# Performance work log

Measured on AMD Instinct MI355X. Metric: run time of the kernel, lower is better.

The kernel has to match this reference:

```python
import jax, jax.numpy as jnp
import numpy as np

B, N, H, V = 64, 640, 768, 50265
LN_EPS = 1e-5


def setup_inputs() -> dict:
    key = jax.random.key(0)
    ks = jax.random.split(key, 12)
    inputs = jax.random.randint(ks[0], (B, N), 0, V)
    position_idx = jax.random.randint(ks[1], (B, N), 0, 10)
    attn_mask = jax.random.randint(ks[2], (B, N, N), 0, 2).astype(bool)
    s = 0.02
    emb_table = jax.random.normal(ks[3], (V, H), jnp.float32) * s
    pooler_w = jax.random.normal(ks[4], (H, H), jnp.float32) * s
    pooler_b = jnp.zeros((H,), jnp.float32)
    dense_w = jax.random.normal(ks[5], (H, H), jnp.float32) * s
    dense_b = jnp.zeros((H,), jnp.float32)
    ln_g = jnp.ones((H,), jnp.float32)
    ln_b = jnp.zeros((H,), jnp.float32)
    dec_w = jax.random.normal(ks[6], (H, 1), jnp.float32) * s
    dec_b = jnp.zeros((1,), jnp.float32)
    return {
        'inputs': inputs, 'position_idx': position_idx, 'attn_mask': attn_mask,
        'emb_table': emb_table, 'pooler_w': pooler_w, 'pooler_b': pooler_b,
        'dense_w': dense_w, 'dense_b': dense_b, 'ln_g': ln_g, 'ln_b': ln_b,
        'dec_w': dec_w, 'dec_b': dec_b,
    }


def _layer_norm(x, g, b):
    mu = jnp.mean(x, axis=-1, keepdims=True)
    var = jnp.mean(jnp.square(x - mu), axis=-1, keepdims=True)
    return (x - mu) * jax.lax.rsqrt(var + LN_EPS) * g + b


def reference(inputs, position_idx, attn_mask, emb_table, pooler_w, pooler_b,
              dense_w, dense_b, ln_g, ln_b, dec_w, dec_b):
    nodes_mask = position_idx == 0            # [B,N] DFG nodes
    token_mask = position_idx >= 2            # [B,N] code tokens
    emb = emb_table[inputs]                   # [B,N,H] word embedding gather
    # node->token adjacency, then row-normalize (broadcast AND fused into float mul)
    m = (nodes_mask[:, :, None] & token_mask[:, None, :] & attn_mask).astype(emb.dtype)
    m = m / (jnp.sum(m, axis=-1, keepdims=True) + 1e-10)
    avg = jnp.einsum('bnm,bmd->bnd', m, emb)  # masked mean of token embs per node
    nm = nodes_mask[:, :, None].astype(emb.dtype)
    emb = emb * (1.0 - nm) + avg * nm
    # encoder stand-in: RoBERTa pooler (dense+tanh on first position) of aggregated embeddings
    pooled = jnp.tanh(emb[:, 0] @ pooler_w + pooler_b)   # [B,H]
    # RobertaLMHead
    x = jax.nn.gelu(pooled @ dense_w + dense_b, approximate=False)
    x = _layer_norm(x, ln_g, ln_b)
    x = x @ dec_w + dec_b                                # [B,1]
    return jnp.tanh(x)
```

## Files before the change

### kernel.cpp

```cpp
#include <hip/hip_runtime.h>
#include <cstdint>

#define B_SZ 64
#define N_SZ 640
#define H_SZ 768
#define NCHUNK 32
#define CHUNK (N_SZ / NCHUNK)
#define LN_EPS 1e-5f

__global__ void k_embed_partial(const int* __restrict__ inputs,
                                const int* __restrict__ pos,
                                const int* __restrict__ amask,
                                const float* __restrict__ emb,
                                float* __restrict__ partials,
                                float* __restrict__ counts) {
    const int c   = blockIdx.x;
    const int b   = blockIdx.y;
    const int tid = threadIdx.x;

    if (pos[b * N_SZ] != 0) return;

    __shared__ float wgt[CHUNK];
    __shared__ int   rowid[CHUNK];
    if (tid < CHUNK) {
        const int m = c * CHUNK + tid;
        const int active = (pos[b * N_SZ + m] >= 2) &&
                           (amask[(size_t)b * N_SZ * N_SZ + m] != 0);
        wgt[tid]   = active ? 1.0f : 0.0f;
        rowid[tid] = inputs[b * N_SZ + m];
    }
    __syncthreads();

    float a0 = 0.f, a1 = 0.f, a2 = 0.f;
#pragma unroll 5
    for (int m = 0; m < CHUNK; ++m) {
        const float  w   = wgt[m];
        const size_t row = (size_t)rowid[m] * H_SZ;
        a0 = fmaf(w, emb[row + tid],       a0);
        a1 = fmaf(w, emb[row + tid + 256], a1);
        a2 = fmaf(w, emb[row + tid + 512], a2);
    }
    float* pout = partials + ((size_t)b * NCHUNK + c) * H_SZ;
    pout[tid]       = a0;
    pout[tid + 256] = a1;
    pout[tid + 512] = a2;
    if (tid == 0) {
        float s = 0.f;
        for (int m = 0; m < CHUNK; ++m) s += wgt[m];
        counts[b * NCHUNK + c] = s;
    }
}

__global__ void k_embed_reduce(const int* __restrict__ inputs,
                               const int* __restrict__ pos,
                               const float* __restrict__ emb,
                               const float* __restrict__ partials,
                               const float* __restrict__ counts,
                               float* __restrict__ e0) {
    const int b   = blockIdx.x;
    const int tid = threadIdx.x;

    if (pos[b * N_SZ] != 0) {
        const size_t row = (size_t)inputs[b * N_SZ] * H_SZ;
        for (int h = tid; h < H_SZ; h += 256)
            e0[b * H_SZ + h] = emb[row + h];
        return;
    }

    float cnt = 0.f;
    for (int c = 0; c < NCHUNK; ++c) cnt += counts[b * NCHUNK + c];
    const float scale = 1.0f / (cnt + 1e-10f);

    float a0 = 0.f, a1 = 0.f, a2 = 0.f;
    const float* p = partials + (size_t)b * NCHUNK * H_SZ;
#pragma unroll 8
    for (int c = 0; c < NCHUNK; ++c) {
        a0 += p[c * H_SZ + tid];
        a1 += p[c * H_SZ + tid + 256];
        a2 += p[c * H_SZ + tid + 512];
    }
    e0[b * H_SZ + tid]       = a0 * scale;
    e0[b * H_SZ + tid + 256] = a1 * scale;
    e0[b * H_SZ + tid + 512] = a2 * scale;
}

template <int ACT>
__global__ void k_gemv(const float* __restrict__ x,
                       const float* __restrict__ w,
                       const float* __restrict__ bias,
                       float* __restrict__ y) {
    const int b = blockIdx.y;
    const int j = blockIdx.x * 256 + threadIdx.x;
    __shared__ float xs[H_SZ];
    for (int h = threadIdx.x; h < H_SZ; h += 256)
        xs[h] = x[b * H_SZ + h];
    __syncthreads();

    float acc = 0.f;
#pragma unroll 8
    for (int k = 0; k < H_SZ; ++k)
        acc = fmaf(xs[k], w[k * H_SZ + j], acc);
    acc += bias[j];
    if (ACT == 0) {
        acc = tanhf(acc);
    } else {
        acc = acc * 0.5f * (1.0f + erff(acc * 0.70710678118654752f));
    }
    y[b * H_SZ + j] = acc;
}

__global__ void k_final(const float* __restrict__ x,
                        const float* __restrict__ g,
                        const float* __restrict__ beta,
                        const float* __restrict__ dw,
                        const float* __restrict__ db,
                        float* __restrict__ out) {
    const int b    = blockIdx.x;
    const int tid  = threadIdx.x;
    const int lane = tid & 63;
    const int wave = tid >> 6;
    __shared__ float red[8];

    const float v0 = x[b * H_SZ + tid];
    const float v1 = x[b * H_SZ + tid + 256];
    const float v2 = x[b * H_SZ + tid + 512];

    float s = v0 + v1 + v2;
    for (int o = 32; o > 0; o >>= 1) s += __shfl_down(s, o, 64);
    if (lane == 0) red[wave] = s;
    __syncthreads();
    if (tid == 0) red[0] = red[0] + red[1] + red[2] + red[3];
    __syncthreads();
    const float mean = red[0] * (1.0f / H_SZ);
    __syncthreads();

    const float d0 = v0 - mean, d1 = v1 - mean, d2 = v2 - mean;
    float q = d0 * d0 + d1 * d1 + d2 * d2;
    for (int o = 32; o > 0; o >>= 1) q += __shfl_down(q, o, 64);
    if (lane == 0) red[wave] = q;
    __syncthreads();
    if (tid == 0) red[0] = red[0] + red[1] + red[2] + red[3];
    __syncthreads();
    const float rstd = rsqrtf(red[0] * (1.0f / H_SZ) + LN_EPS);
    __syncthreads();

    float p = 0.f;
    p += (d0 * rstd * g[tid]       + beta[tid])       * dw[tid];
    p += (d1 * rstd * g[tid + 256] + beta[tid + 256]) * dw[tid + 256];
    p += (d2 * rstd * g[tid + 512] + beta[tid + 512]) * dw[tid + 512];
    for (int o = 32; o > 0; o >>= 1) p += __shfl_down(p, o, 64);
    if (lane == 0) red[wave] = p;
    __syncthreads();
    if (tid == 0)
        out[b] = tanhf(red[0] + red[1] + red[2] + red[3] + db[0]);
}

extern "C" void kernel_launch(void* const* d_in, const int* in_sizes, int n_in,
                              void* d_out, int out_size, void* d_ws, size_t ws_size,
                              hipStream_t stream) {
    const int*   inputs = (const int*)d_in[0];
    const int*   pos    = (const int*)d_in[1];
    const int*   amask  = (const int*)d_in[2];
    const float* emb    = (const float*)d_in[3];
    const float* pw     = (const float*)d_in[4];
    const float* pb     = (const float*)d_in[5];
    const float* dw     = (const float*)d_in[6];
    const float* db     = (const float*)d_in[7];
    const float* lg     = (const float*)d_in[8];
    const float* lb     = (const float*)d_in[9];
    const float* decw   = (const float*)d_in[10];
    const float* decb   = (const float*)d_in[11];
    float* out = (float*)d_out;

    float* partials = (float*)d_ws;
    float* counts   = partials + (size_t)B_SZ * NCHUNK * H_SZ;
    float* e0       = counts + B_SZ * NCHUNK;
    float* pooled   = e0 + B_SZ * H_SZ;
    float* xb       = pooled + B_SZ * H_SZ;

    k_embed_partial<<<dim3(NCHUNK, B_SZ), 256, 0, stream>>>(inputs, pos, amask, emb,
                                                            partials, counts);
    k_embed_reduce<<<B_SZ, 256, 0, stream>>>(inputs, pos, emb, partials, counts, e0);
    k_gemv<0><<<dim3(3, B_SZ), 256, 0, stream>>>(e0, pw, pb, pooled);
    k_gemv<1><<<dim3(3, B_SZ), 256, 0, stream>>>(pooled, dw, db, xb);
    k_final<<<B_SZ, 256, 0, stream>>>(xb, lg, lb, decw, decb, out);
}
```

Before: 94.23 us.

## Fuse embed-reduce into pooler, fuse GELU-GEMV with LayerNorm head, batch two rows per block

```diff
diff --git a/kernel.cpp b/kernel.cpp
--- a/kernel.cpp
+++ b/kernel.cpp
@@ -32,7 +32,7 @@
     __syncthreads();
 
     float a0 = 0.f, a1 = 0.f, a2 = 0.f;
-#pragma unroll 5
+#pragma unroll 10
     for (int m = 0; m < CHUNK; ++m) {
         const float  w   = wgt[m];
         const size_t row = (size_t)rowid[m] * H_SZ;
@@ -51,108 +51,119 @@
     }
 }
 
-__global__ void k_embed_reduce(const int* __restrict__ inputs,
-                               const int* __restrict__ pos,
-                               const float* __restrict__ emb,
-                               const float* __restrict__ partials,
-                               const float* __restrict__ counts,
-                               float* __restrict__ e0) {
-    const int b   = blockIdx.x;
-    const int tid = threadIdx.x;
-
-    if (pos[b * N_SZ] != 0) {
-        const size_t row = (size_t)inputs[b * N_SZ] * H_SZ;
-        for (int h = tid; h < H_SZ; h += 256)
-            e0[b * H_SZ + h] = emb[row + h];
-        return;
+__device__ __forceinline__ float2 block_sum2(float2 v, float2* red2, int tid) {
+    const int lane = tid & 63;
+    const int wave = tid >> 6;
+    for (int o = 32; o > 0; o >>= 1) {
+        v.x += __shfl_down(v.x, o, 64);
+        v.y += __shfl_down(v.y, o, 64);
     }
-
-    float cnt = 0.f;
-    for (int c = 0; c < NCHUNK; ++c) cnt += counts[b * NCHUNK + c];
-    const float scale = 1.0f / (cnt + 1e-10f);
-
-    float a0 = 0.f, a1 = 0.f, a2 = 0.f;
-    const float* p = partials + (size_t)b * NCHUNK * H_SZ;
-#pragma unroll 8
-    for (int c = 0; c < NCHUNK; ++c) {
-        a0 += p[c * H_SZ + tid];
-        a1 += p[c * H_SZ + tid + 256];
-        a2 += p[c * H_SZ + tid + 512];
+    if (lane == 0) red2[wave] = v;
+    __syncthreads();
+    if (tid == 0) {
+        float2 s = make_float2(0.f, 0.f);
+        for (int i = 0; i < 12; ++i) { s.x += red2[i].x; s.y += red2[i].y; }
+        red2[0] = s;
     }
-    e0[b * H_SZ + tid]       = a0 * scale;
-    e0[b * H_SZ + tid + 256] = a1 * scale;
-    e0[b * H_SZ + tid + 512] = a2 * scale;
+    __syncthreads();
+    const float2 s = red2[0];
+    __syncthreads();
+    return s;
 }
 
-template <int ACT>
-__global__ void k_gemv(const float* __restrict__ x,
-                       const float* __restrict__ w,
-                       const float* __restrict__ bias,
-                       float* __restrict__ y) {
-    const int b = blockIdx.y;
-    const int j = blockIdx.x * 256 + threadIdx.x;
-    __shared__ float xs[H_SZ];
-    for (int h = threadIdx.x; h < H_SZ; h += 256)
-        xs[h] = x[b * H_SZ + h];
+__global__ __launch_bounds__(768) void k_pooler(const int* __restrict__ inputs,
+                                                const int* __restrict__ pos,
+                                                const float* __restrict__ emb,
+                                                const float* __restrict__ partials,
+                                                const float* __restrict__ counts,
+                                                const float* __restrict__ pw,
+                                                const float* __restrict__ pb,
+                                                float* __restrict__ pooled) {
+    const int b0 = blockIdx.x * 2;
+    const int j  = threadIdx.x;
+    __shared__ float2 xs[H_SZ];
+
+    float v[2];
+#pragma unroll
+    for (int p = 0; p < 2; ++p) {
+        const int b = b0 + p;
+        if (pos[b * N_SZ] != 0) {
+            v[p] = emb[(size_t)inputs[b * N_SZ] * H_SZ + j];
+        } else {
+            float cnt = 0.f;
+            for (int c = 0; c < NCHUNK; ++c) cnt += counts[b * NCHUNK + c];
+            const float scale = 1.0f / (cnt + 1e-10f);
+            float a = 0.f;
+            const float* pp = partials + (size_t)b * NCHUNK * H_SZ + j;
+#pragma unroll 8
+            for (int c = 0; c < NCHUNK; ++c) a += pp[(size_t)c * H_SZ];
+            v[p] = a * scale;
+        }
+    }
+    xs[j] = make_float2(v[0], v[1]);
     __syncthreads();
 
-    float acc = 0.f;
+    float acc0 = 0.f, acc1 = 0.f;
 #pragma unroll 8
-    for (int k = 0; k < H_SZ; ++k)
-        acc = fmaf(xs[k], w[k * H_SZ + j], acc);
-    acc += bias[j];
-    if (ACT == 0) {
-        acc = tanhf(acc);
-    } else {
-        acc = acc * 0.5f * (1.0f + erff(acc * 0.70710678118654752f));
+    for (int k = 0; k < H_SZ; ++k) {
+        const float  wv = pw[k * H_SZ + j];
+        const float2 xv = xs[k];
+        acc0 = fmaf(wv, xv.x, acc0);
+        acc1 = fmaf(wv, xv.y, acc1);
     }
-    y[b * H_SZ + j] = acc;
+    const float bj = pb[j];
+    pooled[(size_t)b0 * H_SZ + j]       = tanhf(acc0 + bj);
+    pooled[(size_t)(b0 + 1) * H_SZ + j] = tanhf(acc1 + bj);
 }
 
-__global__ void k_final(const float* __restrict__ x,
-                        const float* __restrict__ g,
-                        const float* __restrict__ beta,
-                        const float* __restrict__ dw,
-                        const float* __restrict__ db,
-                        float* __restrict__ out) {
-    const int b    = blockIdx.x;
-    const int tid  = threadIdx.x;
-    const int lane = tid & 63;
-    const int wave = tid >> 6;
-    __shared__ float red[8];
+__global__ __launch_bounds__(768) void k_lmhead(const float* __restrict__ pooled,
+                                                const float* __restrict__ dwm,
+                                                const float* __restrict__ dbv,
+                                                const float* __restrict__ lg,
+                                                const float* __restrict__ lb,
+                                                const float* __restrict__ decw,
+                                                const float* __restrict__ decb,
+                                                float* __restrict__ out) {
+    const int b0 = blockIdx.x * 2;
+    const int j  = threadIdx.x;
+    __shared__ float2 xs[H_SZ];
+    __shared__ float2 red2[12];
 
-    const float v0 = x[b * H_SZ + tid];
-    const float v1 = x[b * H_SZ + tid + 256];
-    const float v2 = x[b * H_SZ + tid + 512];
-
-    float s = v0 + v1 + v2;
-    for (int o = 32; o > 0; o >>= 1) s += __shfl_down(s, o, 64);
-    if (lane == 0) red[wave] = s;
-    __syncthreads();
-    if (tid == 0) red[0] = red[0] + red[1] + red[2] + red[3];
-    __syncthreads();
-    const float mean = red[0] * (1.0f / H_SZ);
+    xs[j] = make_float2(pooled[(size_t)b0 * H_SZ + j],
+                        pooled[(size_t)(b0 + 1) * H_SZ + j]);
     __syncthreads();
 
-    const float d0 = v0 - mean, d1 = v1 - mean, d2 = v2 - mean;
-    float q = d0 * d0 + d1 * d1 + d2 * d2;
-    for (int o = 32; o > 0; o >>= 1) q += __shfl_down(q, o, 64);
-    if (lane == 0) red[wave] = q;
-    __syncthreads();
-    if (tid == 0) red[0] = red[0] + red[1] + red[2] + red[3];
-    __syncthreads();
-    const float rstd = rsqrtf(red[0] * (1.0f / H_SZ) + LN_EPS);
+    float acc0 = 0.f, acc1 = 0.f;
+#pragma unroll 8
+    for (int k = 0; k < H_SZ; ++k) {
+        const float  wv = dwm[k * H_SZ + j];
+        const float2 xv = xs[k];
+        acc0 = fmaf(wv, xv.x, acc0);
+        acc1 = fmaf(wv, xv.y, acc1);
+    }
+    const float bj = dbv[j];
+    acc0 += bj; acc1 += bj;
+    const float g0 = acc0 * 0.5f * (1.0f + erff(acc0 * 0.70710678118654752f));
+    const float g1 = acc1 * 0.5f * (1.0f + erff(acc1 * 0.70710678118654752f));
     __syncthreads();
 
-    float p = 0.f;
-    p += (d0 * rstd * g[tid]       + beta[tid])       * dw[tid];
-    p += (d1 * rstd * g[tid + 256] + beta[tid + 256]) * dw[tid + 256];
-    p += (d2 * rstd * g[tid + 512] + beta[tid + 512]) * dw[tid + 512];
-    for (int o = 32; o > 0; o >>= 1) p += __shfl_down(p, o, 64);
-    if (lane == 0) red[wave] = p;
-    __syncthreads();
-    if (tid == 0)
-        out[b] = tanhf(red[0] + red[1] + red[2] + red[3] + db[0]);
+    const float2 sum = block_sum2(make_float2(g0, g1), red2, j);
+    const float mean0 = sum.x * (1.0f / H_SZ);
+    const float mean1 = sum.y * (1.0f / H_SZ);
+    const float d0 = g0 - mean0, d1 = g1 - mean1;
+    const float2 qs = block_sum2(make_float2(d0 * d0, d1 * d1), red2, j);
+    const float rstd0 = rsqrtf(qs.x * (1.0f / H_SZ) + LN_EPS);
+    const float rstd1 = rsqrtf(qs.y * (1.0f / H_SZ) + LN_EPS);
+
+    const float gj = lg[j], betaj = lb[j], dj = decw[j];
+    const float p0 = (d0 * rstd0 * gj + betaj) * dj;
+    const float p1 = (d1 * rstd1 * gj + betaj) * dj;
+    const float2 dot = block_sum2(make_float2(p0, p1), red2, j);
+    if (j == 0) {
+        const float dbias = decb[0];
+        out[b0]     = tanhf(dot.x + dbias);
+        out[b0 + 1] = tanhf(dot.y + dbias);
+    }
 }
 
 extern "C" void kernel_launch(void* const* d_in, const int* in_sizes, int n_in,
@@ -174,14 +185,11 @@
 
     float* partials = (float*)d_ws;
     float* counts   = partials + (size_t)B_SZ * NCHUNK * H_SZ;
-    float* e0       = counts + B_SZ * NCHUNK;
-    float* pooled   = e0 + B_SZ * H_SZ;
-    float* xb       = pooled + B_SZ * H_SZ;
+    float* pooled   = counts + B_SZ * NCHUNK;
 
     k_embed_partial<<<dim3(NCHUNK, B_SZ), 256, 0, stream>>>(inputs, pos, amask, emb,
                                                             partials, counts);
-    k_embed_reduce<<<B_SZ, 256, 0, stream>>>(inputs, pos, emb, partials, counts, e0);
-    k_gemv<0><<<dim3(3, B_SZ), 256, 0, stream>>>(e0, pw, pb, pooled);
-    k_gemv<1><<<dim3(3, B_SZ), 256, 0, stream>>>(pooled, dw, db, xb);
-    k_final<<<B_SZ, 256, 0, stream>>>(xb, lg, lb, decw, decb, out);
+    k_pooler<<<B_SZ / 2, 768, 0, stream>>>(inputs, pos, emb, partials, counts,
+                                           pw, pb, pooled);
+    k_lmhead<<<B_SZ / 2, 768, 0, stream>>>(pooled, dw, db, lg, lb, decw, decb, out);
 }
```

New measurement: 91.89 us. 2.5% less time.
